# Performance work log

Hardware: AMD Instinct MI355X
Metric: run time of the kernel (lower is better)

The kernel has to match this reference:

```python
import jax, jax.numpy as jnp
import numpy as np

# Room-class id -> type code: ids 0..6 are 'separate' (living_room, kitchen, bedroom,
# missing, balcony, corridor, dining_room) -> code 0; ids 7,8 are 'flexible'
# (bathroom, laundry_room) -> code 1; id 9 is 'affiliated' (closet) -> code 2.
N_SEPARATE = 7
N_FLEXIBLE = 2


def setup_inputs() -> dict:
    key = jax.random.key(0)
    k1, k2 = jax.random.split(key)
    b, n, h, w = 32, 64, 128, 128
    masks = jax.random.normal(k1, (b, n, h, w), dtype=jnp.float32)
    nodes = jax.random.randint(k2, (n,), 0, N_SEPARATE + N_FLEXIBLE + 1, dtype=jnp.int64)
    return {"masks": masks, "nodes": nodes}


def _node_type(nodes):
    # 0 = separate, 1 = flexible, 2 = affiliated
    return jnp.where(nodes < N_SEPARATE, 0, jnp.where(nodes < N_SEPARATE + N_FLEXIBLE, 1, 2))


def reference(masks, nodes):
    b, n, h, w = masks.shape
    m = jnp.clip((masks + 1.0) / 2.0, 0.0, None).reshape(b, n, h * w)  # (b,n,hw)

    # Pairwise overlap Gram matrix and per-node mass sums
    gram = jnp.einsum("bik,bjk->bij", m, m)          # (b,n,n)  sum(mi*mj)
    s = m.sum(axis=-1)                                # (b,n)
    min_s = jnp.minimum(s[:, :, None], s[:, None, :]) # (b,n,n)
    cr = (gram / min_s).mean(axis=0)                  # (n,n) mean over batch

    # Static per-pair beta / skip logic from node types
    t = _node_type(nodes)                             # (n,)
    ti, tj = t[:, None], t[None, :]
    has_f = (ti == 1) | (tj == 1)
    has_a = (ti == 2) | (tj == 2)
    include = ~(has_f & ~has_a)                       # skip 'fs' and 'ff'
    beta = ((ti == 2) ^ (tj == 2)).astype(cr.dtype)   # 1 for 'as'/'af', 0 for 'ss'/'aa'

    triu = jnp.triu(jnp.ones((n, n), dtype=bool), k=1)
    wgt = (include & triu).astype(cr.dtype)
    loss = jnp.sum(jnp.abs(beta - cr) * wgt) / jnp.sum(wgt)
    return loss
```

## Files before the change

### kernel.cpp

```cpp
#include <hip/hip_runtime.h>
#include <cstdint>
#include <cstddef>

static constexpr int HW_ = 16384;
static constexpr int NB_ = 32;
static constexpr int NN_ = 64;
static constexpr int BK_ = 64;

typedef short bfrag  __attribute__((ext_vector_type(8)));
typedef float f32x4  __attribute__((ext_vector_type(4)));

__device__ __forceinline__ unsigned short f2bf_rne(float x) {
    unsigned u = __builtin_bit_cast(unsigned, x);
    return (unsigned short)((u + 0x7FFFu + ((u >> 16) & 1u)) >> 16);
}

__device__ __forceinline__ int swz(int row, int k) {
    int byte = (row << 7) + (k << 1);
    byte ^= (row & 7) << 4;
    return byte >> 1;
}

__global__ __launch_bounds__(256) void gram_kernel(const float* __restrict__ masks,
                                                   float* __restrict__ gram_part,
                                                   float* __restrict__ s_part,
                                                   int NC, int KC) {
    __shared__ __align__(16) unsigned short lds[2][NN_ * BK_];
    const int bx = blockIdx.x;
    const int b  = bx / NC;
    const int c  = bx - b * NC;
    const int t  = threadIdx.x;
    const int l  = t & 63;
    const int w  = t >> 6;
    const int lrow = t >> 4;
    const int lk4  = t & 15;
    const float* mb = masks + (size_t)b * (NN_ * HW_) + (size_t)c * KC;
    const int NT = KC / BK_;

    f32x4 acc[4];
#pragma unroll
    for (int cb = 0; cb < 4; ++cb) acc[cb] = (f32x4){0.f, 0.f, 0.f, 0.f};
    float sreg[4] = {0.f, 0.f, 0.f, 0.f};
    float4 ld[4];

    auto stage_load = [&](int tt) {
        const float* src = mb + tt * BK_ + lk4 * 4;
#pragma unroll
        for (int p = 0; p < 4; ++p)
            ld[p] = *reinterpret_cast<const float4*>(src + (size_t)(lrow + 16 * p) * HW_);
    };
    auto stage_write = [&](unsigned short* buf) {
#pragma unroll
        for (int p = 0; p < 4; ++p) {
            const float m0 = fmaxf(0.f, (ld[p].x + 1.f) * 0.5f);
            const float m1 = fmaxf(0.f, (ld[p].y + 1.f) * 0.5f);
            const float m2 = fmaxf(0.f, (ld[p].z + 1.f) * 0.5f);
            const float m3 = fmaxf(0.f, (ld[p].w + 1.f) * 0.5f);
            sreg[p] += (m0 + m1) + (m2 + m3);
            const ushort4 pk = make_ushort4(f2bf_rne(m0), f2bf_rne(m1),
                                            f2bf_rne(m2), f2bf_rne(m3));
            *reinterpret_cast<ushort4*>(&buf[swz(lrow + 16 * p, lk4 * 4)]) = pk;
        }
    };
    auto compute = [&](const unsigned short* buf) {
#pragma unroll
        for (int ks = 0; ks < BK_; ks += 32) {
            const int kb = ks + ((l >> 4) << 3);
            const bfrag a = *reinterpret_cast<const bfrag*>(&buf[swz((w << 4) + (l & 15), kb)]);
#pragma unroll
            for (int cb = 0; cb < 4; ++cb) {
                const bfrag bb = *reinterpret_cast<const bfrag*>(&buf[swz((cb << 4) + (l & 15), kb)]);
                acc[cb] = __builtin_amdgcn_mfma_f32_16x16x32_bf16(a, bb, acc[cb], 0, 0, 0);
            }
        }
    };

    stage_load(0);
    stage_write(lds[0]);
    __syncthreads();
    for (int tt = 0; tt < NT; ++tt) {
        const int cur = tt & 1;
        const bool more = (tt + 1 < NT);
        if (more) stage_load(tt + 1);
        compute(lds[cur]);
        if (more) stage_write(lds[cur ^ 1]);
        __syncthreads();
    }

    float* gp = gram_part + (size_t)(c * NB_ + b) * (NN_ * NN_);
#pragma unroll
    for (int cb = 0; cb < 4; ++cb)
#pragma unroll
        for (int r = 0; r < 4; ++r) {
            const int i = (w << 4) + ((l >> 4) << 2) + r;
            const int j = (cb << 4) + (l & 15);
            gp[i * NN_ + j] = acc[cb][r];
        }
#pragma unroll
    for (int p = 0; p < 4; ++p) {
        float v = sreg[p];
        v += __shfl_xor(v, 1, 64);
        v += __shfl_xor(v, 2, 64);
        v += __shfl_xor(v, 4, 64);
        v += __shfl_xor(v, 8, 64);
        if ((l & 15) == 0)
            s_part[(size_t)c * (NB_ * NN_) + b * NN_ + (lrow + 16 * p)] = v;
    }
}

__global__ __launch_bounds__(256) void cr_weight_kernel(const float* __restrict__ gram_part,
                                                        const float* __restrict__ s_part,
                                                        float* __restrict__ wq, int NC) {
    __shared__ float s_loc[NN_];
    const int b = blockIdx.x;
    if (threadIdx.x < NN_) {
        float v = 0.f;
        for (int c = 0; c < NC; ++c)
            v += s_part[(size_t)c * (NB_ * NN_) + b * NN_ + threadIdx.x];
        s_loc[threadIdx.x] = v;
    }
    __syncthreads();
    const int ij = blockIdx.y * 256 + threadIdx.x;
    float g = 0.f;
#pragma unroll 8
    for (int c = 0; c < NC; ++c)
        g += gram_part[(size_t)(c * NB_ + b) * (NN_ * NN_) + ij];
    const int i = ij >> 6, j = ij & 63;
    wq[(size_t)b * (NN_ * NN_) + ij] = g / fminf(s_loc[i], s_loc[j]);
}

__global__ __launch_bounds__(256) void loss2_kernel(const float* __restrict__ wq,
                                                    const int* __restrict__ nodes,
                                                    float* __restrict__ num_part,
                                                    float* __restrict__ den_part,
                                                    unsigned int* __restrict__ counter,
                                                    float* __restrict__ out) {
    __shared__ float red[8];
    __shared__ int is_last;
    const int ij = blockIdx.x * 256 + threadIdx.x;
    float acc = 0.f;
#pragma unroll
    for (int b = 0; b < NB_; ++b)
        acc += wq[(size_t)b * (NN_ * NN_) + ij];
    const float cr = acc * (1.0f / NB_);

    const int i = ij >> 6, j = ij & 63;
    const int ni = nodes[i];
    const int nj = nodes[j];
    const int ti = (ni < 7) ? 0 : ((ni < 9) ? 1 : 2);
    const int tj = (nj < 7) ? 0 : ((nj < 9) ? 1 : 2);
    const bool has_f = (ti == 1) || (tj == 1);
    const bool has_a = (ti == 2) || (tj == 2);
    const bool include = !(has_f && !has_a);
    const float beta = ((ti == 2) != (tj == 2)) ? 1.f : 0.f;
    const float wgt = (include && (j > i)) ? 1.f : 0.f;

    float num = wgt * fabsf(beta - cr);
    float den = wgt;
#pragma unroll
    for (int off = 32; off >= 1; off >>= 1) {
        num += __shfl_xor(num, off, 64);
        den += __shfl_xor(den, off, 64);
    }
    const int wave = threadIdx.x >> 6;
    const int lane = threadIdx.x & 63;
    if (lane == 0) { red[wave] = num; red[4 + wave] = den; }
    __syncthreads();
    if (threadIdx.x == 0) {
        const float bn = red[0] + red[1] + red[2] + red[3];
        const float bd = red[4] + red[5] + red[6] + red[7];
        __hip_atomic_store(&num_part[blockIdx.x], bn, __ATOMIC_RELAXED, __HIP_MEMORY_SCOPE_AGENT);
        __hip_atomic_store(&den_part[blockIdx.x], bd, __ATOMIC_RELAXED, __HIP_MEMORY_SCOPE_AGENT);
        const unsigned old = __hip_atomic_fetch_add(counter, 1u, __ATOMIC_ACQ_REL,
                                                    __HIP_MEMORY_SCOPE_AGENT);
        is_last = (old == (unsigned)(gridDim.x - 1));
    }
    __syncthreads();
    if (is_last && threadIdx.x < 64) {
        const int t = threadIdx.x;
        float n16 = 0.f, d16 = 0.f;
        if (t < 16) {
            n16 = __hip_atomic_load(&num_part[t], __ATOMIC_RELAXED, __HIP_MEMORY_SCOPE_AGENT);
            d16 = __hip_atomic_load(&den_part[t], __ATOMIC_RELAXED, __HIP_MEMORY_SCOPE_AGENT);
        }
#pragma unroll
        for (int off = 8; off >= 1; off >>= 1) {
            n16 += __shfl_xor(n16, off, 64);
            d16 += __shfl_xor(d16, off, 64);
        }
        if (t == 0) out[0] = n16 / d16;
    }
}

extern "C" void kernel_launch(void* const* d_in, const int* in_sizes, int n_in,
                              void* d_out, int out_size, void* d_ws, size_t ws_size,
                              hipStream_t stream) {
    const float* masks = (const float*)d_in[0];
    const int* nodes = (const int*)d_in[1];
    float* out = (float*)d_out;

    const size_t ws_floats = ws_size / sizeof(float);
    int NC = 16;
    while (NC > 1) {
        const size_t need = (size_t)NC * NB_ * NN_ * NN_
                          + (size_t)NC * NB_ * NN_
                          + (size_t)NB_ * NN_ * NN_
                          + 2 * 16 + 4;
        if (need <= ws_floats) break;
        NC >>= 1;
    }
    const int KC = HW_ / NC;

    float* gram_part = (float*)d_ws;
    float* s_part    = gram_part + (size_t)NC * NB_ * NN_ * NN_;
    float* wq        = s_part    + (size_t)NC * NB_ * NN_;
    float* num_part  = wq        + (size_t)NB_ * NN_ * NN_;
    float* den_part  = num_part  + 16;
    unsigned int* counter = (unsigned int*)(den_part + 16);

    hipMemsetAsync(counter, 0, sizeof(unsigned int), stream);
    gram_kernel<<<NB_ * NC, 256, 0, stream>>>(masks, gram_part, s_part, NC, KC);
    cr_weight_kernel<<<dim3(NB_, (NN_ * NN_) / 256), 256, 0, stream>>>(gram_part, s_part, wq, NC);
    loss2_kernel<<<(NN_ * NN_) / 256, 256, 0, stream>>>(wq, nodes, num_part, den_part, counter, out);
}
```

Baseline: 42.40 us.

## Fuse cr and loss kernels via atomic counters, drop memset, double-buffer loads

Merges the per-batch ratio kernel and the loss reduction kernel into one epilogue kernel. A per-column-chunk atomic counter lets the last batch block for each chunk do the mean over the batch and the loss, so one launch is removed. The separate hipMemsetAsync is dropped; counter zeroing moves into the first block of the gram kernel. The gram main loop is also unrolled by two with separate register load buffers so global loads run further ahead of compute, at the cost of more registers. The epilogue reads wq values written by other blocks after an acq_rel fetch_add and now uses plain loads for num_part/den_part, which relies on device-scope memory ordering.

Measured after the change: 48.32 us. +14.0%, slower.

```diff
diff --git a/kernel.cpp b/kernel.cpp
--- a/kernel.cpp
+++ b/kernel.cpp
@@ -24,7 +24,10 @@
 __global__ __launch_bounds__(256) void gram_kernel(const float* __restrict__ masks,
                                                    float* __restrict__ gram_part,
                                                    float* __restrict__ s_part,
+                                                   unsigned int* __restrict__ counters,
                                                    int NC, int KC) {
+    if (blockIdx.x == 0 && threadIdx.x < 17) counters[threadIdx.x] = 0u;
+
     __shared__ __align__(16) unsigned short lds[2][NN_ * BK_];
     const int bx = blockIdx.x;
     const int b  = bx / NC;
@@ -41,15 +44,15 @@
 #pragma unroll
     for (int cb = 0; cb < 4; ++cb) acc[cb] = (f32x4){0.f, 0.f, 0.f, 0.f};
     float sreg[4] = {0.f, 0.f, 0.f, 0.f};
-    float4 ld[4];
-
-    auto stage_load = [&](int tt) {
+    float4 ldA[4], ldB[4];
+
+    auto stage_load = [&](float4* ld, int tt) {
         const float* src = mb + tt * BK_ + lk4 * 4;
 #pragma unroll
         for (int p = 0; p < 4; ++p)
             ld[p] = *reinterpret_cast<const float4*>(src + (size_t)(lrow + 16 * p) * HW_);
     };
-    auto stage_write = [&](unsigned short* buf) {
+    auto stage_write = [&](unsigned short* buf, const float4* ld) {
 #pragma unroll
         for (int p = 0; p < 4; ++p) {
             const float m0 = fmaxf(0.f, (ld[p].x + 1.f) * 0.5f);
@@ -75,16 +78,21 @@
         }
     };
 
-    stage_load(0);
-    stage_write(lds[0]);
-    __syncthreads();
-    for (int tt = 0; tt < NT; ++tt) {
-        const int cur = tt & 1;
-        const bool more = (tt + 1 < NT);
-        if (more) stage_load(tt + 1);
-        compute(lds[cur]);
-        if (more) stage_write(lds[cur ^ 1]);
+    stage_load(ldA, 0);
+    stage_write(lds[0], ldA);
+    if (NT > 1) stage_load(ldB, 1);
+    __syncthreads();
+    for (int tt = 0; tt < NT; tt += 2) {
+        if (tt + 2 < NT) stage_load(ldA, tt + 2);
+        if (tt + 1 < NT) stage_write(lds[1], ldB);
+        compute(lds[0]);
         __syncthreads();
+        if (tt + 1 < NT) {
+            if (tt + 3 < NT) stage_load(ldB, tt + 3);
+            if (tt + 2 < NT) stage_write(lds[0], ldA);
+            compute(lds[1]);
+            __syncthreads();
+        }
     }
 
     float* gp = gram_part + (size_t)(c * NB_ + b) * (NN_ * NN_);
@@ -108,43 +116,51 @@
     }
 }
 
-__global__ __launch_bounds__(256) void cr_weight_kernel(const float* __restrict__ gram_part,
-                                                        const float* __restrict__ s_part,
-                                                        float* __restrict__ wq, int NC) {
+__global__ __launch_bounds__(256) void epilogue_kernel(const float* __restrict__ gram_part,
+                                                       const float* __restrict__ s_part,
+                                                       const int* __restrict__ nodes,
+                                                       float* __restrict__ wq,
+                                                       float* __restrict__ num_part,
+                                                       float* __restrict__ den_part,
+                                                       unsigned int* __restrict__ counters,
+                                                       float* __restrict__ out, int NC) {
     __shared__ float s_loc[NN_];
-    const int b = blockIdx.x;
-    if (threadIdx.x < NN_) {
+    __shared__ float red[8];
+    __shared__ int flag;
+    const int b   = blockIdx.x;
+    const int ijc = blockIdx.y;
+    const int t   = threadIdx.x;
+    const int ij  = ijc * 256 + t;
+
+    if (t < NN_) {
         float v = 0.f;
         for (int c = 0; c < NC; ++c)
-            v += s_part[(size_t)c * (NB_ * NN_) + b * NN_ + threadIdx.x];
-        s_loc[threadIdx.x] = v;
-    }
-    __syncthreads();
-    const int ij = blockIdx.y * 256 + threadIdx.x;
+            v += s_part[(size_t)c * (NB_ * NN_) + b * NN_ + t];
+        s_loc[t] = v;
+    }
+    __syncthreads();
     float g = 0.f;
 #pragma unroll 8
     for (int c = 0; c < NC; ++c)
         g += gram_part[(size_t)(c * NB_ + b) * (NN_ * NN_) + ij];
     const int i = ij >> 6, j = ij & 63;
     wq[(size_t)b * (NN_ * NN_) + ij] = g / fminf(s_loc[i], s_loc[j]);
-}
-
-__global__ __launch_bounds__(256) void loss2_kernel(const float* __restrict__ wq,
-                                                    const int* __restrict__ nodes,
-                                                    float* __restrict__ num_part,
-                                                    float* __restrict__ den_part,
-                                                    unsigned int* __restrict__ counter,
-                                                    float* __restrict__ out) {
-    __shared__ float red[8];
-    __shared__ int is_last;
-    const int ij = blockIdx.x * 256 + threadIdx.x;
+
+    __syncthreads();
+    if (t == 0) {
+        const unsigned old = __hip_atomic_fetch_add(&counters[ijc], 1u, __ATOMIC_ACQ_REL,
+                                                    __HIP_MEMORY_SCOPE_AGENT);
+        flag = (old == (unsigned)(NB_ - 1));
+    }
+    __syncthreads();
+    if (!flag) return;
+
     float acc = 0.f;
 #pragma unroll
-    for (int b = 0; b < NB_; ++b)
-        acc += wq[(size_t)b * (NN_ * NN_) + ij];
+    for (int b2 = 0; b2 < NB_; ++b2)
+        acc += wq[(size_t)b2 * (NN_ * NN_) + ij];
     const float cr = acc * (1.0f / NB_);
 
-    const int i = ij >> 6, j = ij & 63;
     const int ni = nodes[i];
     const int nj = nodes[j];
     const int ti = (ni < 7) ? 0 : ((ni < 9) ? 1 : 2);
@@ -162,27 +178,21 @@
         num += __shfl_xor(num, off, 64);
         den += __shfl_xor(den, off, 64);
     }
-    const int wave = threadIdx.x >> 6;
-    const int lane = threadIdx.x & 63;
+    const int wave = t >> 6;
+    const int lane = t & 63;
     if (lane == 0) { red[wave] = num; red[4 + wave] = den; }
     __syncthreads();
-    if (threadIdx.x == 0) {
-        const float bn = red[0] + red[1] + red[2] + red[3];
-        const float bd = red[4] + red[5] + red[6] + red[7];
-        __hip_atomic_store(&num_part[blockIdx.x], bn, __ATOMIC_RELAXED, __HIP_MEMORY_SCOPE_AGENT);
-        __hip_atomic_store(&den_part[blockIdx.x], bd, __ATOMIC_RELAXED, __HIP_MEMORY_SCOPE_AGENT);
-        const unsigned old = __hip_atomic_fetch_add(counter, 1u, __ATOMIC_ACQ_REL,
+    if (t == 0) {
+        num_part[ijc] = red[0] + red[1] + red[2] + red[3];
+        den_part[ijc] = red[4] + red[5] + red[6] + red[7];
+        const unsigned old = __hip_atomic_fetch_add(&counters[16], 1u, __ATOMIC_ACQ_REL,
                                                     __HIP_MEMORY_SCOPE_AGENT);
-        is_last = (old == (unsigned)(gridDim.x - 1));
-    }
-    __syncthreads();
-    if (is_last && threadIdx.x < 64) {
-        const int t = threadIdx.x;
-        float n16 = 0.f, d16 = 0.f;
-        if (t < 16) {
-            n16 = __hip_atomic_load(&num_part[t], __ATOMIC_RELAXED, __HIP_MEMORY_SCOPE_AGENT);
-            d16 = __hip_atomic_load(&den_part[t], __ATOMIC_RELAXED, __HIP_MEMORY_SCOPE_AGENT);
-        }
+        flag = (old == 15u);
+    }
+    __syncthreads();
+    if (flag && t < 64) {
+        float n16 = (t < 16) ? num_part[t] : 0.f;
+        float d16 = (t < 16) ? den_part[t] : 0.f;
 #pragma unroll
         for (int off = 8; off >= 1; off >>= 1) {
             n16 += __shfl_xor(n16, off, 64);
@@ -205,7 +215,7 @@
         const size_t need = (size_t)NC * NB_ * NN_ * NN_
                           + (size_t)NC * NB_ * NN_
                           + (size_t)NB_ * NN_ * NN_
-                          + 2 * 16 + 4;
+                          + 2 * 16 + 17;
         if (need <= ws_floats) break;
         NC >>= 1;
     }
@@ -216,10 +226,9 @@
     float* wq        = s_part    + (size_t)NC * NB_ * NN_;
     float* num_part  = wq        + (size_t)NB_ * NN_ * NN_;
     float* den_part  = num_part  + 16;
-    unsigned int* counter = (unsigned int*)(den_part + 16);
-
-    hipMemsetAsync(counter, 0, sizeof(unsigned int), stream);
-    gram_kernel<<<NB_ * NC, 256, 0, stream>>>(masks, gram_part, s_part, NC, KC);
-    cr_weight_kernel<<<dim3(NB_, (NN_ * NN_) / 256), 256, 0, stream>>>(gram_part, s_part, wq, NC);
-    loss2_kernel<<<(NN_ * NN_) / 256, 256, 0, stream>>>(wq, nodes, num_part, den_part, counter, out);
-}
+    unsigned int* counters = (unsigned int*)(den_part + 16);
+
+    gram_kernel<<<NB_ * NC, 256, 0, stream>>>(masks, gram_part, s_part, counters, NC, KC);
+    epilogue_kernel<<<dim3(NB_, (NN_ * NN_) / 256), 256, 0, stream>>>(
+        gram_part, s_part, nodes, wq, num_part, den_part, counters, out, NC);
+}
```
